# Optimization experiments

Measured on AMD Instinct MI355X. Metric: run time of the kernel, lower is better.

Reference implementation:

```python
import jax, jax.numpy as jnp
import numpy as np

BN_EPS = 1e-5


def setup_inputs() -> dict:
    key = jax.random.key(0)
    ks = jax.random.split(key, 16)
    B, n, m, C1, C2 = 8, 8192, 2048, 256, 256
    Cin, H1, H2 = C1 + C2, 512, 512
    inp = {
        'unknown': jax.random.uniform(ks[0], (B, n, 3), jnp.float32),
        'known': jax.random.uniform(ks[1], (B, m, 3), jnp.float32),
        'unknow_feats': jax.random.normal(ks[2], (B, C1, n), jnp.float32),
        'known_feats': jax.random.normal(ks[3], (B, C2, m), jnp.float32),
        # shared-MLP layer 1: Conv2d(512 -> 512, k=1, bias=False) + BN + ReLU
        'W1': jax.random.normal(ks[4], (H1, Cin), jnp.float32) * (1.0 / np.sqrt(Cin)),
        'g1': jax.random.uniform(ks[5], (H1,), jnp.float32, 0.5, 1.5),
        'b1': jax.random.normal(ks[6], (H1,), jnp.float32) * 0.1,
        'm1': jax.random.normal(ks[7], (H1,), jnp.float32) * 0.1,
        'v1': jax.random.uniform(ks[8], (H1,), jnp.float32, 0.5, 1.5),
        # shared-MLP layer 2
        'W2': jax.random.normal(ks[9], (H2, H1), jnp.float32) * (1.0 / np.sqrt(H1)),
        'g2': jax.random.uniform(ks[10], (H2,), jnp.float32, 0.5, 1.5),
        'b2': jax.random.normal(ks[11], (H2,), jnp.float32) * 0.1,
        'm2': jax.random.normal(ks[12], (H2,), jnp.float32) * 0.1,
        'v2': jax.random.uniform(ks[13], (H2,), jnp.float32, 0.5, 1.5),
    }
    return inp


def three_nn(unknown, known):
    # brute-force squared L2 distances (CUDA kernel returns squared dists)
    d2 = jnp.sum((unknown[:, :, None, :] - known[:, None, :, :]) ** 2, axis=-1)  # (B,n,m)
    neg_d, idx = jax.lax.top_k(-d2, 3)  # 3 smallest
    return -neg_d, idx  # (B,n,3), (B,n,3)


def three_interpolate(feats, idx, weight):
    # feats (B,C,m), idx (B,n,3), weight (B,n,3) -> (B,C,n)
    def _one(f, i, w):
        return jnp.einsum('cnk,nk->cn', f[:, i], w)
    return jax.vmap(_one)(feats, idx, weight)


def _conv_bn_relu(x, W, g, b, mu, var):
    # x (B,Cin,n) -> (B,Cout,n); 1x1 conv + inference BatchNorm + ReLU
    y = jnp.einsum('oc,bcn->bon', W, x)
    scale = g / jnp.sqrt(var + BN_EPS)
    y = y * scale[None, :, None] + (b - mu * scale)[None, :, None]
    return jax.nn.relu(y)


def reference(unknown, known, unknow_feats, known_feats,
              W1, g1, b1, m1, v1, W2, g2, b2, m2, v2):
    dist, idx = three_nn(unknown, known)
    dist_recip = 1.0 / (dist + 1e-8)
    weight = dist_recip / jnp.sum(dist_recip, axis=2, keepdims=True)
    new_features = three_interpolate(known_feats, idx, weight)  # (B,C2,n)
    new_features = jnp.concatenate([new_features, unknow_feats], axis=1)  # (B,C1+C2,n)
    h = _conv_bn_relu(new_features, W1, g1, b1, m1, v1)
    out = _conv_bn_relu(h, W2, g2, b2, m2, v2)
    return out  # (B, 512, n)
```

## Files before the change

kernel.cpp:

```cpp
#include <hip/hip_runtime.h>

typedef __bf16 bf16_t;
typedef __bf16 bf16x8 __attribute__((ext_vector_type(8)));
typedef float f32x4 __attribute__((ext_vector_type(4)));

#define AS1 __attribute__((address_space(1)))
#define AS3 __attribute__((address_space(3)))

__device__ __forceinline__ void gload_lds16(const void* g, void* l) {
    __builtin_amdgcn_global_load_lds((const AS1 unsigned int*)g,
                                     (AS3 unsigned int*)l, 16, 0, 0);
}

__device__ __forceinline__ unsigned int pack2(float a, float b) {
    unsigned short lo = __builtin_bit_cast(unsigned short, (bf16_t)a);
    unsigned short hi = __builtin_bit_cast(unsigned short, (bf16_t)b);
    return (unsigned int)lo | ((unsigned int)hi << 16);
}

__global__ __launch_bounds__(256) void conv_w(const float* W, bf16_t* dst) {
    size_t i = (size_t)blockIdx.x * 256 + threadIdx.x;
    dst[i] = (bf16_t)W[i];
}

__global__ __launch_bounds__(512) void bn_prep(
    const float* g1, const float* b1, const float* m1, const float* v1,
    const float* g2, const float* b2, const float* m2, const float* v2,
    float* s1, float* t1, float* s2, float* t2)
{
    int i = threadIdx.x;
    if (i < 512) {
        float s = __fdiv_rn(g1[i], __fsqrt_rn(__fadd_rn(v1[i], 1e-5f)));
        s1[i] = s;
        t1[i] = __fsub_rn(b1[i], __fmul_rn(m1[i], s));
        float q = __fdiv_rn(g2[i], __fsqrt_rn(__fadd_rn(v2[i], 1e-5f)));
        s2[i] = q;
        t2[i] = __fsub_rn(b2[i], __fmul_rn(m2[i], q));
    }
}

__device__ __forceinline__ void insdi(float d, int i,
                                      float& D1, int& I1, float& D2, int& I2,
                                      float& D3, int& I3) {
    bool q1 = d < D1, q2 = d < D2, q3 = d < D3;
    D3 = q2 ? D2 : (q3 ? d : D3);  I3 = q2 ? I2 : (q3 ? i : I3);
    D2 = q1 ? D1 : (q2 ? d : D2);  I2 = q1 ? I1 : (q2 ? i : I2);
    D1 = q1 ? d : D1;              I1 = q1 ? i : I1;
}

__global__ __launch_bounds__(256) void knn3_kernel(
    const float* __restrict__ unknown, const float* __restrict__ known,
    int* __restrict__ idx3, float* __restrict__ w3)
{
    __shared__ float4 kp[2048];
    __shared__ float md[4][64][3];
    __shared__ int   mi[4][64][3];
    const int b = blockIdx.y;
    const int tid = threadIdx.x;
    const int lane = tid & 63;
    const int wv = tid >> 6;
    const size_t kb = (size_t)b * 2048 * 3;
    for (int t = tid; t < 2048; t += 256) {
        kp[t] = make_float4(known[kb + t * 3 + 0], known[kb + t * 3 + 1],
                            known[kb + t * 3 + 2], 0.f);
    }
    __syncthreads();

    const int p = blockIdx.x * 64 + lane;
    const size_t qo = ((size_t)b * 8192 + p) * 3;
    const float qx = unknown[qo + 0];
    const float qy = unknown[qo + 1];
    const float qz = unknown[qo + 2];

    float d1[4], d2[4], d3[4];
    int   i1[4], i2[4], i3[4];
#pragma unroll
    for (int c = 0; c < 4; ++c) {
        d1[c] = 1e30f; d2[c] = 1e30f; d3[c] = 1e30f;
        i1[c] = 0;     i2[c] = 0;     i3[c] = 0;
    }

    const int jb = wv * 512;
#pragma unroll 2
    for (int t = 0; t < 128; ++t) {
#pragma unroll
        for (int c = 0; c < 4; ++c) {
            const int j = jb + c * 128 + t;
            float4 k = kp[j];
            float dx = __fsub_rn(qx, k.x);
            float dy = __fsub_rn(qy, k.y);
            float dz = __fsub_rn(qz, k.z);
            float d = __fadd_rn(__fadd_rn(__fmul_rn(dx, dx), __fmul_rn(dy, dy)),
                                __fmul_rn(dz, dz));
            insdi(d, j, d1[c], i1[c], d2[c], i2[c], d3[c], i3[c]);
        }
    }
    float D1 = d1[0], D2 = d2[0], D3 = d3[0];
    int   I1 = i1[0], I2 = i2[0], I3 = i3[0];
#pragma unroll
    for (int c = 1; c < 4; ++c) {
        insdi(d1[c], i1[c], D1, I1, D2, I2, D3, I3);
        insdi(d2[c], i2[c], D1, I1, D2, I2, D3, I3);
        insdi(d3[c], i3[c], D1, I1, D2, I2, D3, I3);
    }
    md[wv][lane][0] = D1; md[wv][lane][1] = D2; md[wv][lane][2] = D3;
    mi[wv][lane][0] = I1; mi[wv][lane][1] = I2; mi[wv][lane][2] = I3;
    __syncthreads();

    if (tid < 64) {
        float F1 = md[0][tid][0], F2 = md[0][tid][1], F3 = md[0][tid][2];
        int   J1 = mi[0][tid][0], J2 = mi[0][tid][1], J3 = mi[0][tid][2];
#pragma unroll
        for (int w = 1; w < 4; ++w) {
            insdi(md[w][tid][0], mi[w][tid][0], F1, J1, F2, J2, F3, J3);
            insdi(md[w][tid][1], mi[w][tid][1], F1, J1, F2, J2, F3, J3);
            insdi(md[w][tid][2], mi[w][tid][2], F1, J1, F2, J2, F3, J3);
        }
        float r1 = __fdiv_rn(1.f, __fadd_rn(F1, 1e-8f));
        float r2 = __fdiv_rn(1.f, __fadd_rn(F2, 1e-8f));
        float r3 = __fdiv_rn(1.f, __fadd_rn(F3, 1e-8f));
        float s = __fadd_rn(__fadd_rn(r1, r2), r3);
        const int pp = blockIdx.x * 64 + tid;
        const size_t o = ((size_t)b * 8192 + pp) * 3;
        idx3[o + 0] = J1; idx3[o + 1] = J2; idx3[o + 2] = J3;
        w3[o + 0] = __fdiv_rn(r1, s);
        w3[o + 1] = __fdiv_rn(r2, s);
        w3[o + 2] = __fdiv_rn(r3, s);
    }
}

__global__ __launch_bounds__(256) void transpose_kf(
    const float* __restrict__ kf, float* __restrict__ kfT)
{
    __shared__ float tile[32][33];
    const int b = blockIdx.z;
    const int m0 = blockIdx.x * 32;
    const int c0 = blockIdx.y * 32;
    const int tx = threadIdx.x & 31;
    const int ty = threadIdx.x >> 5;
#pragma unroll
    for (int k = 0; k < 4; ++k) {
        const int c = c0 + ty + k * 8;
        tile[ty + k * 8][tx] = kf[((size_t)b * 256 + c) * 2048 + m0 + tx];
    }
    __syncthreads();
#pragma unroll
    for (int k = 0; k < 4; ++k) {
        const int m = m0 + ty + k * 8;
        kfT[((size_t)b * 2048 + m) * 256 + c0 + tx] = tile[tx][ty + k * 8];
    }
}

__global__ __launch_bounds__(256) void interp_gather(
    const float* __restrict__ kfT, const int* __restrict__ idx3,
    const float* __restrict__ w3, bf16_t* __restrict__ XT,
    int b0, int p0, int P)
{
    const int bl = blockIdx.y;
    const int bg = b0 + bl;
    const int pt = blockIdx.x * 16 + (threadIdx.x >> 4);
    const int ch = (threadIdx.x & 15) * 16;
    const int p = p0 + pt;

    const size_t ib = ((size_t)bg * 8192 + p) * 3;
    const int i0 = idx3[ib + 0] & 2047;
    const int i1 = idx3[ib + 1] & 2047;
    const int i2 = idx3[ib + 2] & 2047;
    const float w0 = w3[ib + 0], w1 = w3[ib + 1], w2 = w3[ib + 2];

    const float4* r0 = (const float4*)(kfT + ((size_t)bg * 2048 + i0) * 256 + ch);
    const float4* r1 = (const float4*)(kfT + ((size_t)bg * 2048 + i1) * 256 + ch);
    const float4* r2 = (const float4*)(kfT + ((size_t)bg * 2048 + i2) * 256 + ch);

    unsigned int u[8];
#pragma unroll
    for (int q = 0; q < 4; ++q) {
        float4 a = r0[q], bv = r1[q], c = r2[q];
        float v0 = w0 * a.x + w1 * bv.x + w2 * c.x;
        float v1 = w0 * a.y + w1 * bv.y + w2 * c.y;
        float v2 = w0 * a.z + w1 * bv.z + w2 * c.z;
        float v3 = w0 * a.w + w1 * bv.w + w2 * c.w;
        u[q * 2 + 0] = pack2(v0, v1);
        u[q * 2 + 1] = pack2(v2, v3);
    }
    uint4* dst = (uint4*)(XT + ((size_t)bl * P + pt) * 512 + ch);
    dst[0] = make_uint4(u[0], u[1], u[2], u[3]);
    dst[1] = make_uint4(u[4], u[5], u[6], u[7]);
}

__global__ __launch_bounds__(256) void uf_transpose(
    const float* __restrict__ uf, bf16_t* __restrict__ XT,
    int b0, int p0, int P)
{
    __shared__ bf16_t tile[64][66];
    const int bl = blockIdx.z;
    const int bg = b0 + bl;
    const int pc = blockIdx.y * 64;
    const int c0 = blockIdx.x * 64;
    const int tid = threadIdx.x;
    const int pl = tid & 63;
    const int grp = tid >> 6;
    const int p = p0 + pc + pl;

#pragma unroll
    for (int cc = 0; cc < 16; ++cc) {
        const int lc = grp * 16 + cc;
        tile[lc][pl] = (bf16_t)uf[((size_t)bg * 256 + c0 + lc) * 8192 + p];
    }
    __syncthreads();

    const int pr = tid >> 2;
    const int cs = (tid & 3) * 16;
    unsigned int u[8];
#pragma unroll
    for (int q = 0; q < 8; ++q) {
        unsigned short lo = __builtin_bit_cast(unsigned short, tile[cs + 2 * q + 0][pr]);
        unsigned short hi = __builtin_bit_cast(unsigned short, tile[cs + 2 * q + 1][pr]);
        u[q] = (unsigned int)lo | ((unsigned int)hi << 16);
    }
    uint4* dst = (uint4*)(XT + ((size_t)bl * P + pc + pr) * 512 + 256 + c0 + cs);
    dst[0] = make_uint4(u[0], u[1], u[2], u[3]);
    dst[1] = make_uint4(u[4], u[5], u[6], u[7]);
}

template <bool CHAN_IS_M, bool F32_OUT>
__global__ __launch_bounds__(256) void gemm_bt_bn_relu(
    const bf16_t* __restrict__ A, const bf16_t* __restrict__ BT,
    void* __restrict__ Cv,
    const float* __restrict__ scale, const float* __restrict__ shift,
    int ldC, size_t strideA, size_t strideB, size_t strideC, size_t cofs)
{
    __shared__ __align__(16) bf16_t As[128 * 32];
    __shared__ __align__(16) bf16_t Bs[128 * 32];

    const int b = blockIdx.z;
    const int m0 = blockIdx.y * 128;
    const int n0 = blockIdx.x * 128;
    const bf16_t* Ab = A + (size_t)b * strideA + (size_t)m0 * 512;
    const bf16_t* Bb = BT + (size_t)b * strideB + (size_t)n0 * 512;
    const size_t cbase = cofs + (size_t)b * strideC;

    const int tid = threadIdx.x;
    const int lane = tid & 63;
    const int wave = tid >> 6;
    const int wm = (wave & 1) * 64;
    const int wn = (wave >> 1) * 64;

    const int ch0 = tid, ch1 = tid + 256;
    const size_t ga0 = (size_t)(ch0 >> 2) * 512 + (size_t)(ch0 & 3) * 8;
    const size_t ga1 = (size_t)(ch1 >> 2) * 512 + (size_t)(ch1 & 3) * 8;

    const int row_a = lane & 15;
    const int koff = (lane >> 4) * 8;

    f32x4 acc[4][4] = {};

    for (int kt = 0; kt < 512; kt += 32) {
        gload_lds16(Ab + ga0 + kt, As + (size_t)ch0 * 8);
        gload_lds16(Ab + ga1 + kt, As + (size_t)ch1 * 8);
        gload_lds16(Bb + ga0 + kt, Bs + (size_t)ch0 * 8);
        gload_lds16(Bb + ga1 + kt, Bs + (size_t)ch1 * 8);
        __builtin_amdgcn_s_waitcnt(0);
        __syncthreads();

        bf16x8 af[4], bfr[4];
#pragma unroll
        for (int i = 0; i < 4; ++i)
            af[i] = *(const bf16x8*)(As + (size_t)(wm + i * 16 + row_a) * 32 + koff);
#pragma unroll
        for (int j = 0; j < 4; ++j)
            bfr[j] = *(const bf16x8*)(Bs + (size_t)(wn + j * 16 + row_a) * 32 + koff);
#pragma unroll
        for (int i = 0; i < 4; ++i)
#pragma unroll
            for (int j = 0; j < 4; ++j)
                acc[i][j] = __builtin_amdgcn_mfma_f32_16x16x32_bf16(
                    af[i], bfr[j], acc[i][j], 0, 0, 0);
        __syncthreads();
    }

    const int col = lane & 15;
    const int rbase = (lane >> 4) * 4;
#pragma unroll
    for (int i = 0; i < 4; ++i) {
#pragma unroll
        for (int j = 0; j < 4; ++j) {
            const int mb = m0 + wm + i * 16 + rbase;
            const int nn = n0 + wn + j * 16 + col;
            float sc = 0.f, sh = 0.f;
            if (!CHAN_IS_M) { sc = scale[nn]; sh = shift[nn]; }
#pragma unroll
            for (int r = 0; r < 4; ++r) {
                const int mm = mb + r;
                float s = CHAN_IS_M ? scale[mm] : sc;
                float t = CHAN_IS_M ? shift[mm] : sh;
                float v = fmaxf(acc[i][j][r] * s + t, 0.0f);
                const size_t ci = cbase + (size_t)mm * (size_t)ldC + nn;
                if (F32_OUT) ((float*)Cv)[ci] = v;
                else         ((bf16_t*)Cv)[ci] = (bf16_t)v;
            }
        }
    }
}

extern "C" void kernel_launch(void* const* d_in, const int* in_sizes, int n_in,
                              void* d_out, int out_size, void* d_ws, size_t ws_size,
                              hipStream_t stream) {
    (void)in_sizes; (void)n_in; (void)out_size;
    const float* unknown  = (const float*)d_in[0];
    const float* known    = (const float*)d_in[1];
    const float* unknow_f = (const float*)d_in[2];
    const float* known_f  = (const float*)d_in[3];
    const float* W1       = (const float*)d_in[4];
    const float* g1 = (const float*)d_in[5]; const float* b1 = (const float*)d_in[6];
    const float* m1 = (const float*)d_in[7]; const float* v1 = (const float*)d_in[8];
    const float* W2       = (const float*)d_in[9];
    const float* g2 = (const float*)d_in[10]; const float* b2 = (const float*)d_in[11];
    const float* m2 = (const float*)d_in[12]; const float* v2 = (const float*)d_in[13];

    char* ws = (char*)d_ws;
    float* s1 = (float*)(ws + 0);
    float* t1 = s1 + 512;
    float* s2 = s1 + 1024;
    float* t2 = s1 + 1536;
    int*    idx3 = (int*)(ws + 16384);
    float*  w3   = (float*)(ws + 16384 + 786432);
    bf16_t* Wc1  = (bf16_t*)(ws + 1589248);
    bf16_t* Wc2  = (bf16_t*)(ws + 2113536);
    float*  kfT  = (float*)(ws + (3u << 20));
    const size_t FIXED = 20u << 20;

    size_t avail = (ws_size > FIXED) ? (ws_size - FIXED) : 0;
    size_t pts = avail / 2048;
    int nb, P;
    if (pts >= 65536)      { nb = 8; P = 8192; }
    else if (pts >= 8192)  { nb = (int)(pts / 8192); P = 8192; }
    else {
        nb = 1;
        P = (int)((pts / 128) * 128);
        if (P < 128) P = 128;
        if (P > 8192) P = 8192;
    }
    bf16_t* XT = (bf16_t*)(ws + FIXED);
    bf16_t* HT = XT + (size_t)nb * P * 512;

    conv_w<<<1024, 256, 0, stream>>>(W1, Wc1);
    conv_w<<<1024, 256, 0, stream>>>(W2, Wc2);
    bn_prep<<<1, 512, 0, stream>>>(g1, b1, m1, v1, g2, b2, m2, v2, s1, t1, s2, t2);
    knn3_kernel<<<dim3(128, 8), 256, 0, stream>>>(unknown, known, idx3, w3);
    transpose_kf<<<dim3(64, 8, 8), 256, 0, stream>>>(known_f, kfT);

    for (int b0 = 0; b0 < 8; b0 += nb) {
        const int cur = (8 - b0 < nb) ? (8 - b0) : nb;
        for (int p0 = 0; p0 < 8192; p0 += P) {
            const int cp = (8192 - p0 < P) ? (8192 - p0) : P;

            interp_gather<<<dim3(cp / 16, cur), 256, 0, stream>>>(
                kfT, idx3, w3, XT, b0, p0, cp);
            uf_transpose<<<dim3(4, cp / 64, cur), 256, 0, stream>>>(
                unknow_f, XT, b0, p0, cp);

            gemm_bt_bn_relu<false, false><<<dim3(4, cp / 128, cur), 256, 0, stream>>>(
                XT, Wc1, HT, s1, t1, 512,
                (size_t)cp * 512, (size_t)0, (size_t)cp * 512, (size_t)0);

            gemm_bt_bn_relu<true, true><<<dim3(cp / 128, 4, cur), 256, 0, stream>>>(
                Wc2, HT, d_out, s2, t2, 8192,
                (size_t)0, (size_t)cp * 512, (size_t)512 * 8192,
                (size_t)b0 * 512 * 8192 + p0);
        }
    }
}
```

Baseline: 431.0 us.

## Merge prep kernels, fuse interp and uf-transpose, stream KNN points from global

Combines the two weight-conversion kernels and the BN prep kernel into one launch. Fuses the interpolation gather and the unknown-feature transpose into one kernel by splitting on block index. In knn3, drops the LDS staging of known points: each wave reads its 512-point slice straight from global memory, where the address is uniform across the wave. The top-3 distance update now uses fmed3/fmin. The aim is fewer launches and less LDS setup and synchronisation, at the risk of wave-uniform global loads being slower than LDS reads in the inner loop.

```diff
diff --git a/kernel.cpp b/kernel.cpp
--- a/kernel.cpp
+++ b/kernel.cpp
@@ -18,53 +18,56 @@
     return (unsigned int)lo | ((unsigned int)hi << 16);
 }
 
-__global__ __launch_bounds__(256) void conv_w(const float* W, bf16_t* dst) {
-    size_t i = (size_t)blockIdx.x * 256 + threadIdx.x;
-    dst[i] = (bf16_t)W[i];
-}
-
-__global__ __launch_bounds__(512) void bn_prep(
+__global__ __launch_bounds__(256) void prep_all(
+    const float* __restrict__ W1, const float* __restrict__ W2,
+    bf16_t* __restrict__ Wc1, bf16_t* __restrict__ Wc2,
     const float* g1, const float* b1, const float* m1, const float* v1,
     const float* g2, const float* b2, const float* m2, const float* v2,
     float* s1, float* t1, float* s2, float* t2)
 {
-    int i = threadIdx.x;
-    if (i < 512) {
-        float s = __fdiv_rn(g1[i], __fsqrt_rn(__fadd_rn(v1[i], 1e-5f)));
-        s1[i] = s;
-        t1[i] = __fsub_rn(b1[i], __fmul_rn(m1[i], s));
-        float q = __fdiv_rn(g2[i], __fsqrt_rn(__fadd_rn(v2[i], 1e-5f)));
-        s2[i] = q;
-        t2[i] = __fsub_rn(b2[i], __fmul_rn(m2[i], q));
+    const int bx = blockIdx.x;
+    if (bx < 1024) {
+        size_t i = (size_t)bx * 256 + threadIdx.x;
+        Wc1[i] = (bf16_t)W1[i];
+    } else if (bx < 2048) {
+        size_t i = (size_t)(bx - 1024) * 256 + threadIdx.x;
+        Wc2[i] = (bf16_t)W2[i];
+    } else {
+#pragma unroll
+        for (int k = 0; k < 2; ++k) {
+            int i = threadIdx.x + k * 256;
+            float s = __fdiv_rn(g1[i], __fsqrt_rn(__fadd_rn(v1[i], 1e-5f)));
+            s1[i] = s;
+            t1[i] = __fsub_rn(b1[i], __fmul_rn(m1[i], s));
+            float q = __fdiv_rn(g2[i], __fsqrt_rn(__fadd_rn(v2[i], 1e-5f)));
+            s2[i] = q;
+            t2[i] = __fsub_rn(b2[i], __fmul_rn(m2[i], q));
+        }
     }
 }
 
 __device__ __forceinline__ void insdi(float d, int i,
                                       float& D1, int& I1, float& D2, int& I2,
                                       float& D3, int& I3) {
-    bool q1 = d < D1, q2 = d < D2, q3 = d < D3;
-    D3 = q2 ? D2 : (q3 ? d : D3);  I3 = q2 ? I2 : (q3 ? i : I3);
-    D2 = q1 ? D1 : (q2 ? d : D2);  I2 = q1 ? I1 : (q2 ? i : I2);
-    D1 = q1 ? d : D1;              I1 = q1 ? i : I1;
+    const bool q1 = d < D1, q2 = d < D2, q3 = d < D3;
+    I3 = q2 ? I2 : (q3 ? i : I3);
+    I2 = q1 ? I1 : (q2 ? i : I2);
+    I1 = q1 ? i : I1;
+    D3 = __builtin_amdgcn_fmed3f(d, D2, D3);
+    D2 = __builtin_amdgcn_fmed3f(d, D1, D2);
+    D1 = fminf(d, D1);
 }
 
 __global__ __launch_bounds__(256) void knn3_kernel(
     const float* __restrict__ unknown, const float* __restrict__ known,
     int* __restrict__ idx3, float* __restrict__ w3)
 {
-    __shared__ float4 kp[2048];
     __shared__ float md[4][64][3];
     __shared__ int   mi[4][64][3];
     const int b = blockIdx.y;
     const int tid = threadIdx.x;
     const int lane = tid & 63;
-    const int wv = tid >> 6;
-    const size_t kb = (size_t)b * 2048 * 3;
-    for (int t = tid; t < 2048; t += 256) {
-        kp[t] = make_float4(known[kb + t * 3 + 0], known[kb + t * 3 + 1],
-                            known[kb + t * 3 + 2], 0.f);
-    }
-    __syncthreads();
+    const int wv = __builtin_amdgcn_readfirstlane(tid >> 6);
 
     const int p = blockIdx.x * 64 + lane;
     const size_t qo = ((size_t)b * 8192 + p) * 3;
@@ -72,6 +75,9 @@
     const float qy = unknown[qo + 1];
     const float qz = unknown[qo + 2];
 
+    const float* kp = known + (size_t)b * 2048 * 3 + (size_t)wv * 512 * 3;
+    const int jb = wv * 512;
+
     float d1[4], d2[4], d3[4];
     int   i1[4], i2[4], i3[4];
 #pragma unroll
@@ -80,19 +86,20 @@
         i1[c] = 0;     i2[c] = 0;     i3[c] = 0;
     }
 
-    const int jb = wv * 512;
 #pragma unroll 2
     for (int t = 0; t < 128; ++t) {
 #pragma unroll
         for (int c = 0; c < 4; ++c) {
-            const int j = jb + c * 128 + t;
-            float4 k = kp[j];
-            float dx = __fsub_rn(qx, k.x);
-            float dy = __fsub_rn(qy, k.y);
-            float dz = __fsub_rn(qz, k.z);
+            const int jl = c * 128 + t;
+            const float kx = kp[jl * 3 + 0];
+            const float ky = kp[jl * 3 + 1];
+            const float kz = kp[jl * 3 + 2];
+            float dx = __fsub_rn(qx, kx);
+            float dy = __fsub_rn(qy, ky);
+            float dz = __fsub_rn(qz, kz);
             float d = __fadd_rn(__fadd_rn(__fmul_rn(dx, dx), __fmul_rn(dy, dy)),
                                 __fmul_rn(dz, dz));
-            insdi(d, j, d1[c], i1[c], d2[c], i2[c], d3[c], i3[c]);
+            insdi(d, jb + jl, d1[c], i1[c], d2[c], i2[c], d3[c], i3[c]);
         }
     }
     float D1 = d1[0], D2 = d2[0], D3 = d3[0];
@@ -151,76 +158,74 @@
     }
 }
 
-__global__ __launch_bounds__(256) void interp_gather(
+__global__ __launch_bounds__(256) void interp_uf(
     const float* __restrict__ kfT, const int* __restrict__ idx3,
-    const float* __restrict__ w3, bf16_t* __restrict__ XT,
-    int b0, int p0, int P)
-{
+    const float* __restrict__ w3, const float* __restrict__ uf,
+    bf16_t* __restrict__ XT, int b0, int p0, int P)
+{
+    __shared__ bf16_t tile[64][66];
     const int bl = blockIdx.y;
     const int bg = b0 + bl;
-    const int pt = blockIdx.x * 16 + (threadIdx.x >> 4);
-    const int ch = (threadIdx.x & 15) * 16;
-    const int p = p0 + pt;
-
-    const size_t ib = ((size_t)bg * 8192 + p) * 3;
-    const int i0 = idx3[ib + 0] & 2047;
-    const int i1 = idx3[ib + 1] & 2047;
-    const int i2 = idx3[ib + 2] & 2047;
-    const float w0 = w3[ib + 0], w1 = w3[ib + 1], w2 = w3[ib + 2];
-
-    const float4* r0 = (const float4*)(kfT + ((size_t)bg * 2048 + i0) * 256 + ch);
-    const float4* r1 = (const float4*)(kfT + ((size_t)bg * 2048 + i1) * 256 + ch);
-    const float4* r2 = (const float4*)(kfT + ((size_t)bg * 2048 + i2) * 256 + ch);
-
-    unsigned int u[8];
-#pragma unroll
-    for (int q = 0; q < 4; ++q) {
-        float4 a = r0[q], bv = r1[q], c = r2[q];
-        float v0 = w0 * a.x + w1 * bv.x + w2 * c.x;
-        float v1 = w0 * a.y + w1 * bv.y + w2 * c.y;
-        float v2 = w0 * a.z + w1 * bv.z + w2 * c.z;
-        float v3 = w0 * a.w + w1 * bv.w + w2 * c.w;
-        u[q * 2 + 0] = pack2(v0, v1);
-        u[q * 2 + 1] = pack2(v2, v3);
-    }
-    uint4* dst = (uint4*)(XT + ((size_t)bl * P + pt) * 512 + ch);
-    dst[0] = make_uint4(u[0], u[1], u[2], u[3]);
-    dst[1] = make_uint4(u[4], u[5], u[6], u[7]);
-}
-
-__global__ __launch_bounds__(256) void uf_transpose(
-    const float* __restrict__ uf, bf16_t* __restrict__ XT,
-    int b0, int p0, int P)
-{
-    __shared__ bf16_t tile[64][66];
-    const int bl = blockIdx.z;
-    const int bg = b0 + bl;
-    const int pc = blockIdx.y * 64;
-    const int c0 = blockIdx.x * 64;
-    const int tid = threadIdx.x;
-    const int pl = tid & 63;
-    const int grp = tid >> 6;
-    const int p = p0 + pc + pl;
-
-#pragma unroll
-    for (int cc = 0; cc < 16; ++cc) {
-        const int lc = grp * 16 + cc;
-        tile[lc][pl] = (bf16_t)uf[((size_t)bg * 256 + c0 + lc) * 8192 + p];
-    }
-    __syncthreads();
-
-    const int pr = tid >> 2;
-    const int cs = (tid & 3) * 16;
-    unsigned int u[8];
-#pragma unroll
-    for (int q = 0; q < 8; ++q) {
-        unsigned short lo = __builtin_bit_cast(unsigned short, tile[cs + 2 * q + 0][pr]);
-        unsigned short hi = __builtin_bit_cast(unsigned short, tile[cs + 2 * q + 1][pr]);
-        u[q] = (unsigned int)lo | ((unsigned int)hi << 16);
-    }
-    uint4* dst = (uint4*)(XT + ((size_t)bl * P + pc + pr) * 512 + 256 + c0 + cs);
-    dst[0] = make_uint4(u[0], u[1], u[2], u[3]);
-    dst[1] = make_uint4(u[4], u[5], u[6], u[7]);
+    const int gsplit = P >> 4;
+
+    if ((int)blockIdx.x < gsplit) {
+        const int pt = blockIdx.x * 16 + (threadIdx.x >> 4);
+        const int ch = (threadIdx.x & 15) * 16;
+        const int p = p0 + pt;
+
+        const size_t ib = ((size_t)bg * 8192 + p) * 3;
+        const int i0 = idx3[ib + 0] & 2047;
+        const int i1 = idx3[ib + 1] & 2047;
+        const int i2 = idx3[ib + 2] & 2047;
+        const float w0 = w3[ib + 0], w1 = w3[ib + 1], w2 = w3[ib + 2];
+
+        const float4* r0 = (const float4*)(kfT + ((size_t)bg * 2048 + i0) * 256 + ch);
+        const float4* r1 = (const float4*)(kfT + ((size_t)bg * 2048 + i1) * 256 + ch);
+        const float4* r2 = (const float4*)(kfT + ((size_t)bg * 2048 + i2) * 256 + ch);
+
+        unsigned int u[8];
+#pragma unroll
+        for (int q = 0; q < 4; ++q) {
+            float4 a = r0[q], bv = r1[q], c = r2[q];
+            float v0 = w0 * a.x + w1 * bv.x + w2 * c.x;
+            float v1 = w0 * a.y + w1 * bv.y + w2 * c.y;
+            float v2 = w0 * a.z + w1 * bv.z + w2 * c.z;
+            float v3 = w0 * a.w + w1 * bv.w + w2 * c.w;
+            u[q * 2 + 0] = pack2(v0, v1);
+            u[q * 2 + 1] = pack2(v2, v3);
+        }
+        uint4* dst = (uint4*)(XT + ((size_t)bl * P + pt) * 512 + ch);
+        dst[0] = make_uint4(u[0], u[1], u[2], u[3]);
+        dst[1] = make_uint4(u[4], u[5], u[6], u[7]);
+    } else {
+        const int u2 = blockIdx.x - gsplit;
+        const int c0 = (u2 & 3) * 64;
+        const int pc = (u2 >> 2) * 64;
+        const int tid = threadIdx.x;
+        const int pl = tid & 63;
+        const int grp = tid >> 6;
+        const int p = p0 + pc + pl;
+
+#pragma unroll
+        for (int cc = 0; cc < 16; ++cc) {
+            const int lc = grp * 16 + cc;
+            tile[lc][pl] = (bf16_t)uf[((size_t)bg * 256 + c0 + lc) * 8192 + p];
+        }
+        __syncthreads();
+
+        const int pr = tid >> 2;
+        const int cs = (tid & 3) * 16;
+        unsigned int u[8];
+#pragma unroll
+        for (int q = 0; q < 8; ++q) {
+            unsigned short lo = __builtin_bit_cast(unsigned short, tile[cs + 2 * q + 0][pr]);
+            unsigned short hi = __builtin_bit_cast(unsigned short, tile[cs + 2 * q + 1][pr]);
+            u[q] = (unsigned int)lo | ((unsigned int)hi << 16);
+        }
+        uint4* dst = (uint4*)(XT + ((size_t)bl * P + pc + pr) * 512 + 256 + c0 + cs);
+        dst[0] = make_uint4(u[0], u[1], u[2], u[3]);
+        dst[1] = make_uint4(u[4], u[5], u[6], u[7]);
+    }
 }
 
 template <bool CHAN_IS_M, bool F32_OUT>
@@ -344,9 +349,9 @@
     bf16_t* XT = (bf16_t*)(ws + FIXED);
     bf16_t* HT = XT + (size_t)nb * P * 512;
 
-    conv_w<<<1024, 256, 0, stream>>>(W1, Wc1);
-    conv_w<<<1024, 256, 0, stream>>>(W2, Wc2);
-    bn_prep<<<1, 512, 0, stream>>>(g1, b1, m1, v1, g2, b2, m2, v2, s1, t1, s2, t2);
+    prep_all<<<2049, 256, 0, stream>>>(W1, W2, Wc1, Wc2,
+                                       g1, b1, m1, v1, g2, b2, m2, v2,
+                                       s1, t1, s2, t2);
     knn3_kernel<<<dim3(128, 8), 256, 0, stream>>>(unknown, known, idx3, w3);
     transpose_kf<<<dim3(64, 8, 8), 256, 0, stream>>>(known_f, kfT);
 
@@ -355,10 +360,8 @@
         for (int p0 = 0; p0 < 8192; p0 += P) {
             const int cp = (8192 - p0 < P) ? (8192 - p0) : P;
 
-            interp_gather<<<dim3(cp / 16, cur), 256, 0, stream>>>(
-                kfT, idx3, w3, XT, b0, p0, cp);
-            uf_transpose<<<dim3(4, cp / 64, cur), 256, 0, stream>>>(
-                unknow_f, XT, b0, p0, cp);
+            interp_uf<<<dim3(cp / 8, cur), 256, 0, stream>>>(
+                kfT, idx3, w3, unknow_f, XT, b0, p0, cp);
 
             gemm_bt_bn_relu<false, false><<<dim3(4, cp / 128, cur), 256, 0, stream>>>(
                 XT, Wc1, HT, s1, t1, 512,
```

Measured after the change: 449.2 us. +4.2%, slower.
